# Performance work log

Measured on AMD Instinct MI355X. Metric: run time of the kernel, lower is better.

## Reference

```python
import jax, jax.numpy as jnp
import numpy as np
from jax import lax

B = 256
C1 = 256          # conv1 channels
NUM_CAPS = 32     # primary capsule types
CAP_DIM = 8       # primary capsule dim
NUM_PRIMARY = NUM_CAPS * 6 * 6  # 1152
NUM_OUT = 10
OUT_DIM = 16
NUM_ROUTING = 3


def squash(v):
    # v: (..., d)
    sq = jnp.sum(v * v, axis=-1, keepdims=True)
    scale = sq / (1.0 + sq)
    return scale * v / jnp.sqrt(sq + 1e-8)


def setup_inputs() -> dict:
    key = jax.random.key(0)
    k = jax.random.split(key, 6)
    x = jax.random.normal(k[0], (B, 1, 28, 28), dtype=jnp.float32)
    # kaiming fan_out init for convs
    conv1_w = jax.random.normal(k[1], (C1, 1, 9, 9), dtype=jnp.float32) * np.sqrt(2.0 / (C1 * 81))
    conv1_b = jnp.zeros((C1,), dtype=jnp.float32)
    pc_out = NUM_CAPS * CAP_DIM  # 256
    pc_w = jax.random.normal(k[2], (pc_out, C1, 9, 9), dtype=jnp.float32) * np.sqrt(2.0 / (pc_out * 81))
    pc_b = jnp.zeros((pc_out,), dtype=jnp.float32)
    W_digit = jax.random.normal(k[3], (NUM_PRIMARY, CAP_DIM, NUM_OUT, OUT_DIM), dtype=jnp.float32) * 0.01
    return {"x": x, "conv1_w": conv1_w, "conv1_b": conv1_b,
            "pc_w": pc_w, "pc_b": pc_b, "W_digit": W_digit}


def _conv(x, w, b, stride):
    y = lax.conv_general_dilated(x, w, (stride, stride), 'VALID',
                                 dimension_numbers=('NCHW', 'OIHW', 'NCHW'))
    return y + b[None, :, None, None]


def reference(x, conv1_w, conv1_b, pc_w, pc_b, W_digit):
    # conv1 + ReLU: (B,1,28,28) -> (B,256,20,20)
    h = jax.nn.relu(_conv(x, conv1_w, conv1_b, 1))
    # primary caps conv: -> (B, 256, 6, 6)
    p = _conv(h, pc_w, pc_b, 2)
    bsz, _, oh, ow = p.shape
    # (B, num_caps, cap_dim, H, W) -> (B, num_caps, H, W, cap_dim) -> (B, N, d)
    p = p.reshape(bsz, NUM_CAPS, CAP_DIM, oh, ow)
    p = jnp.transpose(p, (0, 1, 3, 4, 2)).reshape(bsz, NUM_CAPS * oh * ow, CAP_DIM)
    u = squash(p)  # (B, 1152, 8)
    # dynamic routing
    u_hat = jnp.einsum('bid,idjo->bijo', u, W_digit)  # (B, 1152, 10, 16)
    b_logits = jnp.zeros((bsz, NUM_PRIMARY, NUM_OUT, 1), dtype=u_hat.dtype)
    v = None
    for it in range(NUM_ROUTING):
        c = jax.nn.softmax(b_logits, axis=2)
        s = jnp.sum(c * u_hat, axis=1)          # (B, 10, 16)
        v = squash(s)
        if it < NUM_ROUTING - 1:
            agreement = jnp.sum(u_hat * v[:, None, :, :], axis=-1, keepdims=True)
            b_logits = b_logits + agreement
    return v
```

## Files before the change

### kernel.cpp

```cpp
#include <hip/hip_runtime.h>
#include <hip/hip_bf16.h>

#define NI 1152

typedef __attribute__((ext_vector_type(8))) _Float16 f16x8;
typedef __attribute__((ext_vector_type(4))) float f32x4;
typedef __attribute__((ext_vector_type(8))) unsigned short u16x8;
typedef __attribute__((ext_vector_type(4))) unsigned short u16x4;

static const size_t UHAT_OFF = 0;
static const size_t W6_OFF   = 0;
static const size_t H3_OFF   = 10747904UL;
static const size_t WT1_OFF  = 63176704UL;
static const size_t PP_OFF   = 63259648UL;
static const size_t U_OFF    = 94371840UL;
static const size_t SP_OFF   = 103809024UL;
static const size_t L_OFF    = 127401984UL;
static const size_t V_OFF    = 139198464UL;

__device__ __forceinline__ unsigned short f2bf(float x) {
    unsigned u = __builtin_bit_cast(unsigned, x);
    u += 0x7fffu + ((u >> 16) & 1u);
    return (unsigned short)(u >> 16);
}
__device__ __forceinline__ float bf2f(unsigned short h) {
    return __builtin_bit_cast(float, (unsigned)h << 16);
}
__device__ __forceinline__ void atomAddF(float* p, float v) {
    __hip_atomic_fetch_add(p, v, __ATOMIC_RELAXED, __HIP_MEMORY_SCOPE_AGENT);
}

__global__ __launch_bounds__(256) void k_prep_w(const float* __restrict__ pcw,
                                                _Float16* __restrict__ w6) {
    __shared__ float sl[5184];
    int oc  = blockIdx.x;
    int ic0 = blockIdx.y * 64;
    const float* src = pcw + (size_t)oc * 20736 + (size_t)ic0 * 81;
    for (int j = threadIdx.x; j < 5184; j += 256) sl[j] = src[j];
    __syncthreads();
    int og = oc >> 4, fr = oc & 15;
    for (int t = threadIdx.x; t < 5184; t += 256) {
        int tap = t >> 6, i = t & 63;
        int ic = ic0 + i;
        int ks = ic >> 5, kch = (ic >> 3) & 3, icl = ic & 7;
        int lane = kch * 16 + fr;
        w6[(((size_t)(tap * 8 + ks) * 16 + og) * 64 + lane) * 8 + icl] =
            (_Float16)sl[i * 81 + tap];
    }
}

__global__ void k_transpose_w1(const float* __restrict__ w, float* __restrict__ wT) {
    int t = blockIdx.x, oc = threadIdx.x;
    wT[t * 256 + oc] = w[oc * 81 + t];
}

__global__ __launch_bounds__(256) void k_conv1(const float* __restrict__ x,
                                               const float* __restrict__ wT1,
                                               const float* __restrict__ bias,
                                               _Float16* __restrict__ h3) {
    __shared__ _Float16 hs[2][20][256];
    int b  = blockIdx.y;
    int rp = blockIdx.x;
    int oc = threadIdx.x;
    int oy0 = rp * 2;
    const float* xb = x + (size_t)b * 784;
    float bv = bias[oc];
    float acc0[20], acc1[20];
#pragma unroll
    for (int i = 0; i < 20; ++i) { acc0[i] = bv; acc1[i] = bv; }
    for (int ky = 0; ky < 9; ++ky) {
        const float* r0 = xb + (oy0 + ky) * 28;
        const float* r1 = r0 + 28;
        float x0[28], x1[28];
#pragma unroll
        for (int c = 0; c < 28; ++c) { x0[c] = r0[c]; x1[c] = r1[c]; }
#pragma unroll
        for (int kx = 0; kx < 9; ++kx) {
            float w = wT1[(ky * 9 + kx) * 256 + oc];
#pragma unroll
            for (int px = 0; px < 20; ++px) {
                acc0[px] += x0[px + kx] * w;
                acc1[px] += x1[px + kx] * w;
            }
        }
    }
#pragma unroll
    for (int px = 0; px < 20; ++px) {
        hs[0][px][oc] = (_Float16)fmaxf(acc0[px], 0.f);
        hs[1][px][oc] = (_Float16)fmaxf(acc1[px], 0.f);
    }
    __syncthreads();
    for (int cid = threadIdx.x; cid < 1280; cid += 256) {
        int kp = cid & 31;
        int pos = cid >> 5;
        int ry = pos / 20, px2 = pos % 20;
        int ks = kp >> 2, p = kp & 3;
        f16x8 val = *(const f16x8*)&hs[ry][px2][ks * 32 + p * 8];
        _Float16* dst = h3 + ((size_t)((ks * 400 + (oy0 + ry) * 20 + px2) * 4 + p) * 256 + b) * 8;
        *(f16x8*)dst = val;
    }
}

__global__ __launch_bounds__(256, 2) void k_conv2_direct(
    const _Float16* __restrict__ h3, const _Float16* __restrict__ w6,
    float* __restrict__ pp) {
    const int mt = blockIdx.x, nt = blockIdx.y, ks = blockIdx.z;
    const int pos = mt >> 1, bhalf = mt & 1;
    const int py = pos / 6, px = pos % 6;
    const int l = threadIdx.x & 63;
    const int w = threadIdx.x >> 6;
    const int wm = w >> 1, wn = w & 1;
    const int p = l >> 4, fr = l & 15;

    const _Float16* abase = h3 + (size_t)ks * 3276800 + p * 2048 +
                            (bhalf * 128 + wm * 64 + fr) * 8;
    const _Float16* bbase = w6 + (nt * 8 + wn * 4) * 512 + l * 8;

    f16x8 a[3][4], b[3][4];
    f32x4 acc[4][4];
    const f32x4 z = {0.f, 0.f, 0.f, 0.f};
#pragma unroll
    for (int mi = 0; mi < 4; ++mi)
#pragma unroll
        for (int ni = 0; ni < 4; ++ni) acc[mi][ni] = z;

#define LOADAB(buf, tap)                                                       \
    do {                                                                       \
        const int _t = (tap);                                                  \
        const int _y = _t / 9, _x = _t - _y * 9;                               \
        const _Float16* _ab = abase + ((2 * py + _y) * 20 + (2 * px + _x)) * 8192; \
        a[buf][0] = *(const f16x8*)(_ab);                                      \
        a[buf][1] = *(const f16x8*)(_ab + 128);                                \
        a[buf][2] = *(const f16x8*)(_ab + 256);                                \
        a[buf][3] = *(const f16x8*)(_ab + 384);                                \
        const _Float16* _bb = bbase + (size_t)(_t * 8 + ks) * 8192;            \
        b[buf][0] = *(const f16x8*)(_bb);                                      \
        b[buf][1] = *(const f16x8*)(_bb + 512);                                \
        b[buf][2] = *(const f16x8*)(_bb + 1024);                               \
        b[buf][3] = *(const f16x8*)(_bb + 1536);                               \
    } while (0)

#define MFMA_ALL(buf)                                                          \
    do {                                                                       \
        _Pragma("unroll") for (int mi = 0; mi < 4; ++mi)                       \
            _Pragma("unroll") for (int ni = 0; ni < 4; ++ni)                   \
                acc[mi][ni] = __builtin_amdgcn_mfma_f32_16x16x32_f16(          \
                    a[buf][mi], b[buf][ni], acc[mi][ni], 0, 0, 0);             \
    } while (0)

    LOADAB(0, 0);
    LOADAB(1, 1);
    for (int k = 0; k < 27; ++k) {
        const int t0 = 3 * k;
        LOADAB(2, t0 + 2);
        MFMA_ALL(0);
        if (t0 + 3 < 81) LOADAB(0, t0 + 3);
        MFMA_ALL(1);
        if (t0 + 4 < 81) LOADAB(1, t0 + 4);
        MFMA_ALL(2);
    }
#undef LOADAB
#undef MFMA_ALL

    const int row0 = (l >> 4) * 4;
    const int ncol = l & 15;
#pragma unroll
    for (int mi = 0; mi < 4; ++mi)
#pragma unroll
        for (int ni = 0; ni < 4; ++ni) {
            int n = nt * 128 + wn * 64 + ni * 16 + ncol;
#pragma unroll
            for (int reg = 0; reg < 4; ++reg) {
                int m = pos * 256 + bhalf * 128 + wm * 64 + mi * 16 + row0 + reg;
                atomAddF(&pp[(size_t)m * 256 + n], acc[mi][ni][reg]);
            }
        }
}

__global__ __launch_bounds__(256) void k_sum_squash2(const float* __restrict__ pp,
                                                     const float* __restrict__ bias,
                                                     float* __restrict__ u) {
    int m = blockIdx.x * 8 + (threadIdx.x >> 5);
    int cap = threadIdx.x & 31;
    const float* p0 = pp + (size_t)m * 256 + cap * 8;
    float s[8], sq = 0.f;
#pragma unroll
    for (int d = 0; d < 8; ++d) {
        float a = p0[d] + bias[cap * 8 + d];
        sq += a * a; s[d] = a;
    }
    float scale = sq / ((1.0f + sq) * sqrtf(sq + 1e-8f));
    int pos = m >> 8, b = m & 255;
    int i = cap * 36 + pos;
    float* up = u + ((size_t)i * 256 + b) * 8;
    ((float4*)up)[0] = make_float4(scale * s[0], scale * s[1], scale * s[2], scale * s[3]);
    ((float4*)up)[1] = make_float4(scale * s[4], scale * s[5], scale * s[6], scale * s[7]);
}

__global__ __launch_bounds__(256) void k_build_uhat(const float* __restrict__ u,
                                                    const float* __restrict__ W,
                                                    unsigned short* __restrict__ UH) {
    __shared__ float Ws[1280];
    int i = blockIdx.x;
    for (int t = threadIdx.x; t < 1280; t += 256) Ws[t] = W[(size_t)i * 1280 + t];
    __syncthreads();
    int b = threadIdx.x;
    const float* uptr = u + ((size_t)i * 256 + b) * 8;
    float u8[8];
    ((float4*)u8)[0] = ((const float4*)uptr)[0];
    ((float4*)u8)[1] = ((const float4*)uptr)[1];
#pragma unroll
    for (int j = 0; j < 10; ++j) {
        float o16[16];
#pragma unroll
        for (int o = 0; o < 16; ++o) o16[o] = 0.f;
#pragma unroll
        for (int d = 0; d < 8; ++d) {
            const float* wp = Ws + d * 160 + j * 16;
#pragma unroll
            for (int o = 0; o < 16; ++o) o16[o] += u8[d] * wp[o];
        }
        u16x8 h0, h1;
#pragma unroll
        for (int o = 0; o < 8; ++o) { h0[o] = f2bf(o16[o]); h1[o] = f2bf(o16[8 + o]); }
        unsigned short* dst = UH + ((size_t)(i * 10 + j) * 256 + b) * 16;
        *(u16x8*)dst = h0;
        *(u16x8*)(dst + 8) = h1;
    }
}

__global__ __launch_bounds__(256) void k_route_s0(const unsigned short* __restrict__ UH,
                                                  float* __restrict__ SP) {
    int it = blockIdx.x, bt = blockIdx.y;
    int b0 = bt * 64, i0 = it * 8;
    int b_l = threadIdx.x & 63;
    int og = __builtin_amdgcn_readfirstlane((int)(threadIdx.x >> 6));
    float acc[10][4];
#pragma unroll
    for (int j = 0; j < 10; ++j)
#pragma unroll
        for (int o = 0; o < 4; ++o) acc[j][o] = 0.f;
    for (int li = 0; li < 8; ++li) {
        const unsigned short* up = UH + ((size_t)(i0 + li) * 10 * 256 + b0 + b_l) * 16 + og * 4;
#pragma unroll
        for (int j = 0; j < 10; ++j) {
            u16x4 t = *(const u16x4*)(up + j * 4096);
#pragma unroll
            for (int o = 0; o < 4; ++o) acc[j][o] += bf2f(t[o]);
        }
    }
    float* sp = SP + ((size_t)it * 256 + b0 + b_l) * 160 + og * 4;
#pragma unroll
    for (int j = 0; j < 10; ++j)
        *(float4*)(sp + j * 16) = make_float4(0.1f * acc[j][0], 0.1f * acc[j][1],
                                              0.1f * acc[j][2], 0.1f * acc[j][3]);
}

__global__ __launch_bounds__(256) void k_route_as(float* __restrict__ L,
                                                  const unsigned short* __restrict__ UH,
                                                  const float* __restrict__ V,
                                                  float* __restrict__ SP,
                                                  int add, int storeL) {
    __shared__ float VL[64][165];
    __shared__ float LG[64][81];
    int it = blockIdx.x, bt = blockIdx.y;
    int b0 = bt * 64, i0 = it * 8;
    int b_l = threadIdx.x & 63;
    int ig = __builtin_amdgcn_readfirstlane((int)(threadIdx.x >> 6));
    int b_r = threadIdx.x >> 2, part = threadIdx.x & 3;
    {
        const float4* vsrc = (const float4*)(V + (size_t)(b0 + b_r) * 160 + part * 40);
#pragma unroll
        for (int q = 0; q < 10; ++q) {
            float4 vv = vsrc[q]; int c = part * 40 + q * 4;
            VL[b_r][c] = vv.x; VL[b_r][c + 1] = vv.y; VL[b_r][c + 2] = vv.z; VL[b_r][c + 3] = vv.w;
        }
        if (add) {
            const float4* lsrc = (const float4*)(L + (size_t)(b0 + b_r) * 11520 + i0 * 10 + part * 20);
#pragma unroll
            for (int q = 0; q < 5; ++q) {
                float4 t = lsrc[q]; int c = part * 20 + q * 4;
                LG[b_r][c] = t.x; LG[b_r][c + 1] = t.y; LG[b_r][c + 2] = t.z; LG[b_r][c + 3] = t.w;
            }
        }
    }
    __syncthreads();
#pragma unroll
    for (int ii = 0; ii < 2; ++ii) {
        int il = ig * 2 + ii;
        int i = i0 + il;
        const unsigned short* up = UH + ((size_t)i * 10 * 256 + b0 + b_l) * 16;
#pragma unroll
        for (int j = 0; j < 10; ++j) {
            u16x8 ua = *(const u16x8*)(up + j * 4096);
            u16x8 ub = *(const u16x8*)(up + j * 4096 + 8);
            float a = 0.f;
#pragma unroll
            for (int o = 0; o < 8; ++o) a += bf2f(ua[o]) * VL[b_l][j * 16 + o];
#pragma unroll
            for (int o = 0; o < 8; ++o) a += bf2f(ub[o]) * VL[b_l][j * 16 + 8 + o];
            float base = add ? LG[b_l][il * 10 + j] : 0.f;
            LG[b_l][il * 10 + j] = base + a;
        }
    }
    __syncthreads();
    if (storeL) {
        float4* ldst = (float4*)(L + (size_t)(b0 + b_r) * 11520 + i0 * 10 + part * 20);
#pragma unroll
        for (int q = 0; q < 5; ++q) {
            int c = part * 20 + q * 4;
            ldst[q] = make_float4(LG[b_r][c], LG[b_r][c + 1], LG[b_r][c + 2], LG[b_r][c + 3]);
        }
    }
    float acc[10][4];
#pragma unroll
    for (int j = 0; j < 10; ++j)
#pragma unroll
        for (int o = 0; o < 4; ++o) acc[j][o] = 0.f;
    for (int li = 0; li < 8; ++li) {
        float lg[10];
#pragma unroll
        for (int j = 0; j < 10; ++j) lg[j] = LG[b_l][li * 10 + j];
        float m = lg[0];
#pragma unroll
        for (int j = 1; j < 10; ++j) m = fmaxf(m, lg[j]);
        float e[10], ssum = 0.f;
#pragma unroll
        for (int j = 0; j < 10; ++j) { e[j] = __expf(lg[j] - m); ssum += e[j]; }
        float inv = 1.0f / ssum;
        const unsigned short* up = UH + ((size_t)(i0 + li) * 10 * 256 + b0 + b_l) * 16 + ig * 4;
#pragma unroll
        for (int j = 0; j < 10; ++j) {
            float cj = e[j] * inv;
            u16x4 t = *(const u16x4*)(up + j * 4096);
#pragma unroll
            for (int o = 0; o < 4; ++o) acc[j][o] += cj * bf2f(t[o]);
        }
    }
    float* sp = SP + ((size_t)it * 256 + b0 + b_l) * 160 + ig * 4;
#pragma unroll
    for (int j = 0; j < 10; ++j)
        *(float4*)(sp + j * 16) = make_float4(acc[j][0], acc[j][1], acc[j][2], acc[j][3]);
}

__global__ __launch_bounds__(256) void k_route_v(const float* __restrict__ SP,
                                                 float* __restrict__ vout) {
    int n = blockIdx.x * 256 + threadIdx.x;
    float ssum = 0.f;
    for (int t = 0; t < 144; ++t) ssum += SP[(size_t)t * 40960 + n];
    float sq = ssum * ssum;
    float tot = sq;
#pragma unroll
    for (int mask = 1; mask < 16; mask <<= 1) tot += __shfl_xor(tot, mask, 64);
    float scale = tot / ((1.0f + tot) * sqrtf(tot + 1e-8f));
    vout[n] = scale * ssum;
}

extern "C" void kernel_launch(void* const* d_in, const int* in_sizes, int n_in,
                              void* d_out, int out_size, void* d_ws, size_t ws_size,
                              hipStream_t stream) {
    (void)in_sizes; (void)n_in; (void)out_size; (void)ws_size;
    const float* x   = (const float*)d_in[0];
    const float* c1w = (const float*)d_in[1];
    const float* c1b = (const float*)d_in[2];
    const float* pcw = (const float*)d_in[3];
    const float* pcb = (const float*)d_in[4];
    const float* Wd  = (const float*)d_in[5];
    float* out = (float*)d_out;
    char* wsb  = (char*)d_ws;

    unsigned short* uh = (unsigned short*)(wsb + UHAT_OFF);
    _Float16* w6 = (_Float16*)(wsb + W6_OFF);
    _Float16* h3 = (_Float16*)(wsb + H3_OFF);
    float* wT1 = (float*)(wsb + WT1_OFF);
    float* pp  = (float*)(wsb + PP_OFF);
    float* u   = (float*)(wsb + U_OFF);
    float* sp  = (float*)(wsb + SP_OFF);
    float* lg  = (float*)(wsb + L_OFF);
    float* v   = (float*)(wsb + V_OFF);

    hipMemsetAsync(pp, 0, (size_t)9216 * 256 * sizeof(float), stream);

    k_prep_w<<<dim3(256, 4), 256, 0, stream>>>(pcw, w6);
    k_transpose_w1<<<81, 256, 0, stream>>>(c1w, wT1);
    k_conv1<<<dim3(10, 256), 256, 0, stream>>>(x, wT1, c1b, h3);
    k_conv2_direct<<<dim3(72, 2, 8), 256, 0, stream>>>(h3, w6, pp);
    k_sum_squash2<<<1152, 256, 0, stream>>>(pp, pcb, u);
    k_build_uhat<<<1152, 256, 0, stream>>>(u, Wd, uh);

    k_route_s0<<<dim3(144, 4), 256, 0, stream>>>(uh, sp);
    k_route_v<<<160, 256, 0, stream>>>(sp, v);
    k_route_as<<<dim3(144, 4), 256, 0, stream>>>(lg, uh, v, sp, 0, 1);
    k_route_v<<<160, 256, 0, stream>>>(sp, v);
    k_route_as<<<dim3(144, 4), 256, 0, stream>>>(lg, uh, v, sp, 1, 0);
    k_route_v<<<160, 256, 0, stream>>>(sp, out);
}
```

Before: 461.9 us.

## Stage conv2 tiles through LDS and fuse squash, u_hat build and first routing sum

The primary-caps conv is restructured so each block covers all 256 batch rows of one output position. A and B tiles are staged in LDS via global_load_lds, two taps per iteration, with a larger 8x4 MFMA accumulator per wave. This halves the grid and raises reuse, but adds two barriers per iteration and zero-pads w6 for the odd last tap. Separately, squash, u_hat construction and the first routing sum are fused into one kernel, removing the u buffer and a re-read of u_hat.

```diff
diff --git a/kernel.cpp b/kernel.cpp
--- a/kernel.cpp
+++ b/kernel.cpp
@@ -10,10 +10,9 @@
 
 static const size_t UHAT_OFF = 0;
 static const size_t W6_OFF   = 0;
-static const size_t H3_OFF   = 10747904UL;
-static const size_t WT1_OFF  = 63176704UL;
-static const size_t PP_OFF   = 63259648UL;
-static const size_t U_OFF    = 94371840UL;
+static const size_t H3_OFF   = 10750976UL;
+static const size_t WT1_OFF  = 63179776UL;
+static const size_t PP_OFF   = 94371840UL;
 static const size_t SP_OFF   = 103809024UL;
 static const size_t L_OFF    = 127401984UL;
 static const size_t V_OFF    = 139198464UL;
@@ -29,6 +28,11 @@
 __device__ __forceinline__ void atomAddF(float* p, float v) {
     __hip_atomic_fetch_add(p, v, __ATOMIC_RELAXED, __HIP_MEMORY_SCOPE_AGENT);
 }
+
+#define GLD16(gsrc, ldst)                                                      \
+    __builtin_amdgcn_global_load_lds(                                          \
+        (__attribute__((address_space(1))) const void*)(gsrc),                 \
+        (__attribute__((address_space(3))) void*)(ldst), 16, 0, 0)
 
 __global__ __launch_bounds__(256) void k_prep_w(const float* __restrict__ pcw,
                                                 _Float16* __restrict__ w6) {
@@ -101,155 +105,123 @@
     }
 }
 
-__global__ __launch_bounds__(256, 2) void k_conv2_direct(
+__global__ __launch_bounds__(256, 2) void k_conv2_mfma(
     const _Float16* __restrict__ h3, const _Float16* __restrict__ w6,
     float* __restrict__ pp) {
-    const int mt = blockIdx.x, nt = blockIdx.y, ks = blockIdx.z;
-    const int pos = mt >> 1, bhalf = mt & 1;
+    __shared__ _Float16 As[16384], Bs[8192];
+    const int pos = blockIdx.x, nt = blockIdx.y, ks = blockIdx.z;
     const int py = pos / 6, px = pos % 6;
     const int l = threadIdx.x & 63;
-    const int w = threadIdx.x >> 6;
+    const int w = __builtin_amdgcn_readfirstlane((int)(threadIdx.x >> 6));
     const int wm = w >> 1, wn = w & 1;
-    const int p = l >> 4, fr = l & 15;
-
-    const _Float16* abase = h3 + (size_t)ks * 3276800 + p * 2048 +
-                            (bhalf * 128 + wm * 64 + fr) * 8;
-    const _Float16* bbase = w6 + (nt * 8 + wn * 4) * 512 + l * 8;
-
-    f16x8 a[3][4], b[3][4];
-    f32x4 acc[4][4];
+    const int kch = l >> 4, fr = l & 15;
+
+    f32x4 acc[8][4];
     const f32x4 z = {0.f, 0.f, 0.f, 0.f};
 #pragma unroll
-    for (int mi = 0; mi < 4; ++mi)
+    for (int mi = 0; mi < 8; ++mi)
 #pragma unroll
         for (int ni = 0; ni < 4; ++ni) acc[mi][ni] = z;
 
-#define LOADAB(buf, tap)                                                       \
-    do {                                                                       \
-        const int _t = (tap);                                                  \
-        const int _y = _t / 9, _x = _t - _y * 9;                               \
-        const _Float16* _ab = abase + ((2 * py + _y) * 20 + (2 * px + _x)) * 8192; \
-        a[buf][0] = *(const f16x8*)(_ab);                                      \
-        a[buf][1] = *(const f16x8*)(_ab + 128);                                \
-        a[buf][2] = *(const f16x8*)(_ab + 256);                                \
-        a[buf][3] = *(const f16x8*)(_ab + 384);                                \
-        const _Float16* _bb = bbase + (size_t)(_t * 8 + ks) * 8192;            \
-        b[buf][0] = *(const f16x8*)(_bb);                                      \
-        b[buf][1] = *(const f16x8*)(_bb + 512);                                \
-        b[buf][2] = *(const f16x8*)(_bb + 1024);                               \
-        b[buf][3] = *(const f16x8*)(_bb + 1536);                               \
-    } while (0)
-
-#define MFMA_ALL(buf)                                                          \
-    do {                                                                       \
-        _Pragma("unroll") for (int mi = 0; mi < 4; ++mi)                       \
-            _Pragma("unroll") for (int ni = 0; ni < 4; ++ni)                   \
-                acc[mi][ni] = __builtin_amdgcn_mfma_f32_16x16x32_f16(          \
-                    a[buf][mi], b[buf][ni], acc[mi][ni], 0, 0, 0);             \
-    } while (0)
-
-    LOADAB(0, 0);
-    LOADAB(1, 1);
-    for (int k = 0; k < 27; ++k) {
-        const int t0 = 3 * k;
-        LOADAB(2, t0 + 2);
-        MFMA_ALL(0);
-        if (t0 + 3 < 81) LOADAB(0, t0 + 3);
-        MFMA_ALL(1);
-        if (t0 + 4 < 81) LOADAB(1, t0 + 4);
-        MFMA_ALL(2);
-    }
-#undef LOADAB
-#undef MFMA_ALL
-
-    const int row0 = (l >> 4) * 4;
-    const int ncol = l & 15;
-#pragma unroll
-    for (int mi = 0; mi < 4; ++mi)
+    const size_t h3base = (size_t)ks * 400 * 8192;
+
+    for (int it = 0; it < 41; ++it) {
+        const int t0 = 2 * it, t1 = t0 + 1;
+        const int tA1 = (t1 > 80) ? 80 : t1;
+#pragma unroll
+        for (int tl = 0; tl < 2; ++tl) {
+            const int tap  = tl ? t1 : t0;
+            const int tapA = tl ? tA1 : t0;
+            const int y = 2 * py + tapA / 9, xx = 2 * px + tapA % 9;
+            const _Float16* asrc = h3 + h3base + (size_t)(y * 20 + xx) * 8192 + w * 2048 + l * 8;
+#pragma unroll
+            for (int q = 0; q < 4; ++q)
+                GLD16(asrc + q * 512, As + tl * 8192 + w * 2048 + q * 512);
+            const _Float16* bsrc = w6 + ((size_t)(tap * 8 + ks) * 16 + nt * 8 + w * 2) * 512 + l * 8;
+            GLD16(bsrc,       Bs + tl * 4096 + w * 1024);
+            GLD16(bsrc + 512, Bs + tl * 4096 + w * 1024 + 512);
+        }
+        __syncthreads();
+#pragma unroll
+        for (int tl = 0; tl < 2; ++tl) {
+            const _Float16* Ab = As + tl * 8192 + kch * 2048 + (wm * 128 + fr) * 8;
+            const _Float16* Bb = Bs + tl * 4096 + wn * 2048 + kch * 128 + fr * 8;
+            f16x8 a[8], b[4];
+#pragma unroll
+            for (int mi = 0; mi < 8; ++mi) a[mi] = *(const f16x8*)(Ab + mi * 128);
+#pragma unroll
+            for (int ni = 0; ni < 4; ++ni) b[ni] = *(const f16x8*)(Bb + ni * 512);
+#pragma unroll
+            for (int mi = 0; mi < 8; ++mi)
+#pragma unroll
+                for (int ni = 0; ni < 4; ++ni)
+                    acc[mi][ni] = __builtin_amdgcn_mfma_f32_16x16x32_f16(a[mi], b[ni], acc[mi][ni], 0, 0, 0);
+        }
+        __syncthreads();
+    }
+    const int row0 = kch * 4;
+#pragma unroll
+    for (int mi = 0; mi < 8; ++mi)
 #pragma unroll
         for (int ni = 0; ni < 4; ++ni) {
-            int n = nt * 128 + wn * 64 + ni * 16 + ncol;
+            int nloc = wn * 64 + ni * 16 + fr;
 #pragma unroll
             for (int reg = 0; reg < 4; ++reg) {
-                int m = pos * 256 + bhalf * 128 + wm * 64 + mi * 16 + row0 + reg;
-                atomAddF(&pp[(size_t)m * 256 + n], acc[mi][ni][reg]);
+                int mloc = wm * 128 + mi * 16 + row0 + reg;
+                atomAddF(&pp[((size_t)pos * 256 + mloc) * 256 + nt * 128 + nloc],
+                         acc[mi][ni][reg]);
             }
         }
 }
 
-__global__ __launch_bounds__(256) void k_sum_squash2(const float* __restrict__ pp,
-                                                     const float* __restrict__ bias,
-                                                     float* __restrict__ u) {
-    int m = blockIdx.x * 8 + (threadIdx.x >> 5);
-    int cap = threadIdx.x & 31;
-    const float* p0 = pp + (size_t)m * 256 + cap * 8;
-    float s[8], sq = 0.f;
-#pragma unroll
-    for (int d = 0; d < 8; ++d) {
-        float a = p0[d] + bias[cap * 8 + d];
-        sq += a * a; s[d] = a;
-    }
-    float scale = sq / ((1.0f + sq) * sqrtf(sq + 1e-8f));
-    int pos = m >> 8, b = m & 255;
-    int i = cap * 36 + pos;
-    float* up = u + ((size_t)i * 256 + b) * 8;
-    ((float4*)up)[0] = make_float4(scale * s[0], scale * s[1], scale * s[2], scale * s[3]);
-    ((float4*)up)[1] = make_float4(scale * s[4], scale * s[5], scale * s[6], scale * s[7]);
-}
-
-__global__ __launch_bounds__(256) void k_build_uhat(const float* __restrict__ u,
-                                                    const float* __restrict__ W,
-                                                    unsigned short* __restrict__ UH) {
-    __shared__ float Ws[1280];
-    int i = blockIdx.x;
-    for (int t = threadIdx.x; t < 1280; t += 256) Ws[t] = W[(size_t)i * 1280 + t];
-    __syncthreads();
-    int b = threadIdx.x;
-    const float* uptr = u + ((size_t)i * 256 + b) * 8;
-    float u8[8];
-    ((float4*)u8)[0] = ((const float4*)uptr)[0];
-    ((float4*)u8)[1] = ((const float4*)uptr)[1];
-#pragma unroll
-    for (int j = 0; j < 10; ++j) {
-        float o16[16];
-#pragma unroll
-        for (int o = 0; o < 16; ++o) o16[o] = 0.f;
-#pragma unroll
-        for (int d = 0; d < 8; ++d) {
-            const float* wp = Ws + d * 160 + j * 16;
-#pragma unroll
-            for (int o = 0; o < 16; ++o) o16[o] += u8[d] * wp[o];
-        }
-        u16x8 h0, h1;
-#pragma unroll
-        for (int o = 0; o < 8; ++o) { h0[o] = f2bf(o16[o]); h1[o] = f2bf(o16[8 + o]); }
-        unsigned short* dst = UH + ((size_t)(i * 10 + j) * 256 + b) * 16;
-        *(u16x8*)dst = h0;
-        *(u16x8*)(dst + 8) = h1;
-    }
-}
-
-__global__ __launch_bounds__(256) void k_route_s0(const unsigned short* __restrict__ UH,
+__global__ __launch_bounds__(256) void k_postconv(const float* __restrict__ pp,
+                                                  const float* __restrict__ bias,
+                                                  const float* __restrict__ W,
+                                                  unsigned short* __restrict__ UH,
                                                   float* __restrict__ SP) {
     int it = blockIdx.x, bt = blockIdx.y;
-    int b0 = bt * 64, i0 = it * 8;
-    int b_l = threadIdx.x & 63;
-    int og = __builtin_amdgcn_readfirstlane((int)(threadIdx.x >> 6));
+    int i0 = it * 8, b0 = bt * 64;
+    int og = threadIdx.x & 3, b_l = threadIdx.x >> 2;
+    int b = b0 + b_l;
     float acc[10][4];
 #pragma unroll
     for (int j = 0; j < 10; ++j)
 #pragma unroll
         for (int o = 0; o < 4; ++o) acc[j][o] = 0.f;
+#pragma unroll
     for (int li = 0; li < 8; ++li) {
-        const unsigned short* up = UH + ((size_t)(i0 + li) * 10 * 256 + b0 + b_l) * 16 + og * 4;
+        int i = i0 + li;
+        int cap = i / 36, posi = i - cap * 36;
+        const float* p0 = pp + ((size_t)posi * 256 + b) * 256 + cap * 8;
+        float4 pa = ((const float4*)p0)[0];
+        float4 pb = ((const float4*)p0)[1];
+        const float* bs = bias + cap * 8;
+        float s8[8] = {pa.x + bs[0], pa.y + bs[1], pa.z + bs[2], pa.w + bs[3],
+                       pb.x + bs[4], pb.y + bs[5], pb.z + bs[6], pb.w + bs[7]};
+        float sq = 0.f;
+#pragma unroll
+        for (int d = 0; d < 8; ++d) sq += s8[d] * s8[d];
+        float scale = sq / ((1.0f + sq) * sqrtf(sq + 1e-8f));
+        float u8[8];
+#pragma unroll
+        for (int d = 0; d < 8; ++d) u8[d] = scale * s8[d];
+        const float* Wi = W + (size_t)i * 1280 + og * 4;
 #pragma unroll
         for (int j = 0; j < 10; ++j) {
-            u16x4 t = *(const u16x4*)(up + j * 4096);
-#pragma unroll
-            for (int o = 0; o < 4; ++o) acc[j][o] += bf2f(t[o]);
-        }
-    }
-    float* sp = SP + ((size_t)it * 256 + b0 + b_l) * 160 + og * 4;
+            float o4[4] = {0.f, 0.f, 0.f, 0.f};
+#pragma unroll
+            for (int d = 0; d < 8; ++d) {
+                float4 wv = *(const float4*)(Wi + d * 160 + j * 16);
+                o4[0] += u8[d] * wv.x; o4[1] += u8[d] * wv.y;
+                o4[2] += u8[d] * wv.z; o4[3] += u8[d] * wv.w;
+            }
+            u16x4 h;
+#pragma unroll
+            for (int o = 0; o < 4; ++o) { h[o] = f2bf(o4[o]); acc[j][o] += o4[o]; }
+            *(u16x4*)(UH + ((size_t)(i * 10 + j) * 256 + b) * 16 + og * 4) = h;
+        }
+    }
+    float* sp = SP + ((size_t)it * 256 + b) * 160 + og * 4;
 #pragma unroll
     for (int j = 0; j < 10; ++j)
         *(float4*)(sp + j * 16) = make_float4(0.1f * acc[j][0], 0.1f * acc[j][1],
@@ -374,21 +346,19 @@
     _Float16* h3 = (_Float16*)(wsb + H3_OFF);
     float* wT1 = (float*)(wsb + WT1_OFF);
     float* pp  = (float*)(wsb + PP_OFF);
-    float* u   = (float*)(wsb + U_OFF);
     float* sp  = (float*)(wsb + SP_OFF);
     float* lg  = (float*)(wsb + L_OFF);
     float* v   = (float*)(wsb + V_OFF);
 
     hipMemsetAsync(pp, 0, (size_t)9216 * 256 * sizeof(float), stream);
+    hipMemsetAsync(w6 + (size_t)81 * 65536, 0, 131072, stream);
 
     k_prep_w<<<dim3(256, 4), 256, 0, stream>>>(pcw, w6);
     k_transpose_w1<<<81, 256, 0, stream>>>(c1w, wT1);
     k_conv1<<<dim3(10, 256), 256, 0, stream>>>(x, wT1, c1b, h3);
-    k_conv2_direct<<<dim3(72, 2, 8), 256, 0, stream>>>(h3, w6, pp);
-    k_sum_squash2<<<1152, 256, 0, stream>>>(pp, pcb, u);
-    k_build_uhat<<<1152, 256, 0, stream>>>(u, Wd, uh);
-
-    k_route_s0<<<dim3(144, 4), 256, 0, stream>>>(uh, sp);
+    k_conv2_mfma<<<dim3(36, 2, 8), 256, 0, stream>>>(h3, w6, pp);
+    k_postconv<<<dim3(144, 4), 256, 0, stream>>>(pp, pcb, Wd, uh, sp);
+
     k_route_v<<<160, 256, 0, stream>>>(sp, v);
     k_route_as<<<dim3(144, 4), 256, 0, stream>>>(lg, uh, v, sp, 0, 1);
     k_route_v<<<160, 256, 0, stream>>>(sp, v);
```

Result: slower. 523.0 us (+13.2%).
